# Optimization experiments

Hardware: AMD Instinct MI355X
Metric: run time of the kernel (lower is better)

Reference implementation:

```python
import jax, jax.numpy as jnp
from jax import lax
import numpy as np

T, IN, H, L = 8192, 128, 1024, 3


def setup_inputs() -> dict:
    key = jax.random.key(0)
    ks = jax.random.split(key, 12)
    s = 0.05  # scale params to avoid saturating sigmoid/tanh
    return {
        "S": jax.random.normal(ks[0], (T, IN), jnp.float32),
        "h0": jax.random.normal(ks[1], (L, H), jnp.float32),
        "w_ih0": jax.random.normal(ks[2], (2 * H, IN), jnp.float32) * s,
        "w_hh0": jax.random.normal(ks[3], (2 * H, H), jnp.float32) * s,
        "b_ih0": jax.random.normal(ks[4], (2 * H,), jnp.float32) * s,
        "b_hh0": jax.random.normal(ks[5], (2 * H,), jnp.float32) * s,
        "w_ih_rest": jax.random.normal(ks[6], (L - 1, 2 * H, H), jnp.float32) * s,
        "w_hh_rest": jax.random.normal(ks[7], (L - 1, 2 * H, H), jnp.float32) * s,
        "b_ih_rest": jax.random.normal(ks[8], (L - 1, 2 * H), jnp.float32) * s,
        "b_hh_rest": jax.random.normal(ks[9], (L - 1, 2 * H), jnp.float32) * s,
        "w_out": jax.random.normal(ks[10], (1, H), jnp.float32) * s,
        "b_out": jax.random.normal(ks[11], (1,), jnp.float32) * s,
    }


def _mgu_layer(x_seq, h0, w_ih, w_hh, b_ih, b_hh):
    # Precompute the input projection for all timesteps at once: [T, 2H]
    gi = x_seq @ w_ih.T + b_ih

    def step(h, gi_t):
        gh = h @ w_hh.T + b_hh                      # [2H]
        i_f, i_n = jnp.split(gi_t, 2)
        h_f, h_n = jnp.split(gh, 2)
        f = jax.nn.sigmoid(i_f + h_f)               # forget gate
        n = jnp.tanh(i_n + f * h_n)                 # new candidate
        hy = n + (1.0 - f) * (h - n)
        return hy, hy

    _, out = lax.scan(step, h0, gi)                 # out: [T, H]
    return out


def reference(S, h0, w_ih0, w_hh0, b_ih0, b_hh0,
              w_ih_rest, w_hh_rest, b_ih_rest, b_hh_rest,
              w_out, b_out):
    x = _mgu_layer(S, h0[0], w_ih0, w_hh0, b_ih0, b_hh0)
    for l in range(w_ih_rest.shape[0]):             # fixed small layer count
        x = _mgu_layer(x, h0[l + 1], w_ih_rest[l], w_hh_rest[l],
                       b_ih_rest[l], b_hh_rest[l])
    out = (x @ w_out.T + b_out).reshape(-1)          # [T]
    return out
```

## Files before the change

### kernel.cpp

```cpp
#include <hip/hip_runtime.h>
#include <math.h>
#include <stdint.h>


#define T_STEPS 8192
#define HDIM 1024
#define RING 128

typedef unsigned long long u64;

__device__ __forceinline__ u64 agload64(const u64* p) {
    return __hip_atomic_load(p, __ATOMIC_RELAXED, __HIP_MEMORY_SCOPE_AGENT);
}
__device__ __forceinline__ void agstore64(u64* p, u64 v) {
    __hip_atomic_store(p, v, __ATOMIC_RELAXED, __HIP_MEMORY_SCOPE_AGENT);
}
__device__ __forceinline__ int agloadi(const int* p) {
    return __hip_atomic_load(p, __ATOMIC_RELAXED, __HIP_MEMORY_SCOPE_AGENT);
}
__device__ __forceinline__ void agstorei(int* p, int v) {
    __hip_atomic_store(p, v, __ATOMIC_RELAXED, __HIP_MEMORY_SCOPE_AGENT);
}
__device__ __forceinline__ float dot4(float4 a, float4 b) {
    return a.x * b.x + a.y * b.y + a.z * b.z + a.w * b.w;
}
__device__ __forceinline__ u64 pack(float v, int tag) {
    return ((u64)(unsigned)tag << 32) | (u64)__float_as_uint(v);
}
__device__ __forceinline__ void opaque4(float4& v) {
    asm volatile("" : "+v"(v.x), "+v"(v.y), "+v"(v.z), "+v"(v.w));
}
__device__ __forceinline__ void opaque2(float2& v) {
    asm volatile("" : "+v"(v.x), "+v"(v.y));
}

template <int K, int L>
__device__ void scan_layer(float* __restrict__ s_h,
                           float* __restrict__ s_x,
                           const float* __restrict__ S,
                           const u64*  __restrict__ xring_in,
                           u64*        __restrict__ xring_out,
                           float*      __restrict__ xout,
                           const float* __restrict__ h0,
                           const float* __restrict__ w_ih,
                           const float* __restrict__ b_ih,
                           const float* __restrict__ w_hh,
                           const float* __restrict__ b_hh,
                           u64* __restrict__ htag,
                           int* __restrict__ progNext,
                           int* __restrict__ progSelf,
                           int r)
{
    const int tid = threadIdx.x;
    const int a   = tid >> 6;
    const int q   = tid & 63;
    const int jb  = r * 16 + 2 * a;

    float4 wf[2][4], wn[2][4];
#pragma unroll
    for (int g = 0; g < 2; ++g) {
        const float* rf = w_hh + (size_t)(jb + g) * HDIM;
        const float* rn = w_hh + (size_t)(HDIM + jb + g) * HDIM;
#pragma unroll
        for (int m = 0; m < 4; ++m) {
            wf[g][m] = *(const float4*)(rf + 4 * q + 256 * m);
            wn[g][m] = *(const float4*)(rn + 4 * q + 256 * m);
            opaque4(wf[g][m]); opaque4(wn[g][m]);
        }
    }
    float4 wif[2][4], win[2][4];
    float2 wif2[2], win2[2];
    if constexpr (K == 1024) {
#pragma unroll
        for (int g = 0; g < 2; ++g) {
            const float* rf = w_ih + (size_t)(jb + g) * K;
            const float* rn = w_ih + (size_t)(HDIM + jb + g) * K;
#pragma unroll
            for (int m = 0; m < 4; ++m) {
                wif[g][m] = *(const float4*)(rf + 4 * q + 256 * m);
                win[g][m] = *(const float4*)(rn + 4 * q + 256 * m);
                opaque4(wif[g][m]); opaque4(win[g][m]);
            }
        }
    } else {
#pragma unroll
        for (int g = 0; g < 2; ++g) {
            wif2[g] = *(const float2*)(w_ih + (size_t)(jb + g) * K + 2 * q);
            win2[g] = *(const float2*)(w_ih + (size_t)(HDIM + jb + g) * K + 2 * q);
            opaque2(wif2[g]); opaque2(win2[g]);
        }
    }
    float bFv[2], bInv[2], bHnv[2];
#pragma unroll
    for (int g = 0; g < 2; ++g) {
        bFv[g]  = b_ih[jb + g] + b_hh[jb + g];
        bInv[g] = b_ih[HDIM + jb + g];
        bHnv[g] = b_hh[HDIM + jb + g];
    }

    int lastProg = 0;
    for (int t = 0; t < T_STEPS; ++t) {
        const int par = t & 1;
        const u64* hrow = htag + (size_t)((t + 1) & 1) * HDIM;
        u64*       hpub = htag + (size_t)par * HDIM;
        float* hD = s_h + par * HDIM;
        float* xD = s_x + par * HDIM;

        if constexpr (L < 2) {
            if (t - lastProg > RING - 16) {
                do { lastProg = agloadi(progNext); } while (t - lastProg > RING - 16);
            }
        }

        if (t == 0) {
            hD[tid]       = h0[tid];
            hD[tid + 512] = h0[tid + 512];
        }
        {
            const unsigned he = (unsigned)t;
            const unsigned xe = (unsigned)(t + 1);
            const u64* xrow = (L > 0)
                ? xring_in + (size_t)(t & (RING - 1)) * HDIM : nullptr;
            u64 hw0 = 0, hw1 = 0, xw0 = 0, xw1 = 0;
            bool d0 = (t == 0), d1 = (t == 0);
            bool e0 = (L == 0), e1 = (L == 0);
            while (!(d0 && d1 && e0 && e1)) {
                if (!d0) { hw0 = agload64(hrow + tid);       d0 = ((unsigned)(hw0 >> 32) == he); }
                if (!d1) { hw1 = agload64(hrow + tid + 512); d1 = ((unsigned)(hw1 >> 32) == he); }
                if constexpr (L > 0) {
                    if (!e0) { xw0 = agload64(xrow + tid);       e0 = ((unsigned)(xw0 >> 32) == xe); }
                    if (!e1) { xw1 = agload64(xrow + tid + 512); e1 = ((unsigned)(xw1 >> 32) == xe); }
                }
            }
            if (t > 0) {
                hD[tid]       = __uint_as_float((unsigned)hw0);
                hD[tid + 512] = __uint_as_float((unsigned)hw1);
            }
            if constexpr (L > 0) {
                xD[tid]       = __uint_as_float((unsigned)xw0);
                xD[tid + 512] = __uint_as_float((unsigned)xw1);
            }
        }
        if constexpr (L == 0) {
            if (tid < K / 4)
                ((float4*)xD)[tid] = ((const float4*)(S + (size_t)t * K))[tid];
        }
        __syncthreads();

        if constexpr (L > 0) {
            if (r == 0 && tid == 0) agstorei(progSelf, t + 1);
        }

        float aF[2]  = {0.f, 0.f};
        float aNh[2] = {0.f, 0.f};
        float aNi[2] = {0.f, 0.f};
#pragma unroll
        for (int m = 0; m < 4; ++m) {
            const float4 h4 = ((const float4*)hD)[q + 64 * m];
#pragma unroll
            for (int g = 0; g < 2; ++g) {
                aF[g]  += dot4(wf[g][m], h4);
                aNh[g] += dot4(wn[g][m], h4);
            }
        }
        if constexpr (K == 1024) {
#pragma unroll
            for (int m = 0; m < 4; ++m) {
                const float4 x4 = ((const float4*)xD)[q + 64 * m];
#pragma unroll
                for (int g = 0; g < 2; ++g) {
                    aF[g]  += dot4(wif[g][m], x4);
                    aNi[g] += dot4(win[g][m], x4);
                }
            }
        } else {
            const float2 x2 = *(const float2*)&xD[2 * q];
#pragma unroll
            for (int g = 0; g < 2; ++g) {
                aF[g]  += wif2[g].x * x2.x + wif2[g].y * x2.y;
                aNi[g] += win2[g].x * x2.x + win2[g].y * x2.y;
            }
        }

#pragma unroll
        for (int g = 0; g < 2; ++g) {
            aF[g]  += __shfl_xor(aF[g],  1, 64);
            aNh[g] += __shfl_xor(aNh[g], 1, 64);
            aNi[g] += __shfl_xor(aNi[g], 1, 64);
        }
        const int gs = q & 1;
        float vF  = gs ? aF[1]  : aF[0];
        float vNh = gs ? aNh[1] : aNh[0];
        float vNi = gs ? aNi[1] : aNi[0];
#pragma unroll
        for (int off = 2; off <= 32; off <<= 1) {
            vF  += __shfl_xor(vF,  off, 64);
            vNh += __shfl_xor(vNh, off, 64);
            vNi += __shfl_xor(vNi, off, 64);
        }

        if (q < 2) {
            const float cF  = gs ? bFv[1]  : bFv[0];
            const float cIn = gs ? bInv[1] : bInv[0];
            const float cHn = gs ? bHnv[1] : bHnv[0];
            const int   j   = jb + q;
            const float hp  = hD[j];
            const float f   = 1.f / (1.f + expf(-(vF + cF)));
            const float n   = tanhf(vNi + cIn + f * (vNh + cHn));
            const float hy  = n + (1.f - f) * (hp - n);
            const u64   pk  = pack(hy, t + 1);
            agstore64(hpub + j, pk);
            if constexpr (L < 2) {
                agstore64(xring_out + (size_t)(t & (RING - 1)) * HDIM + j, pk);
            } else {
                xout[(size_t)t * HDIM + j] = hy;
            }
        }
    }
}

__global__ __launch_bounds__(512, 2)
void mgu_pipe(const float* __restrict__ S,
              const float* __restrict__ h0,
              const float* __restrict__ w_ih0, const float* __restrict__ b_ih0,
              const float* __restrict__ w_hh0, const float* __restrict__ b_hh0,
              const float* __restrict__ w_ih_r, const float* __restrict__ b_ih_r,
              const float* __restrict__ w_hh_r, const float* __restrict__ b_hh_r,
              float* __restrict__ xbuf2, u64* __restrict__ ring0,
              u64* __restrict__ ring1, u64* __restrict__ htag,
              int* __restrict__ prog)
{
    __shared__ __align__(16) float s_h[2 * HDIM];
    __shared__ __align__(16) float s_x[2 * HDIM];
    const int grp = blockIdx.x >> 6;
    const int r   = blockIdx.x & 63;
    if (grp == 0) {
        scan_layer<128, 0>(s_h, s_x, S, nullptr, ring0, nullptr, h0,
                           w_ih0, b_ih0, w_hh0, b_hh0,
                           htag, prog + 1, nullptr, r);
    } else if (grp == 1) {
        scan_layer<1024, 1>(s_h, s_x, nullptr, ring0, ring1, nullptr, h0 + HDIM,
                            w_ih_r, b_ih_r, w_hh_r, b_hh_r,
                            htag + 2 * HDIM, prog + 2, prog + 1, r);
    } else {
        scan_layer<1024, 2>(s_h, s_x, nullptr, ring1, nullptr, xbuf2,
                            h0 + 2 * HDIM,
                            w_ih_r + 2048 * 1024, b_ih_r + 2048,
                            w_hh_r + 2048 * 1024, b_hh_r + 2048,
                            htag + 4 * HDIM, nullptr, prog + 2, r);
    }
}

__global__ __launch_bounds__(256)
void mgu_out(const float* __restrict__ x,
             const float* __restrict__ w_out,
             const float* __restrict__ b_out,
             float* __restrict__ out)
{
    const int wave = threadIdx.x >> 6;
    const int lane = threadIdx.x & 63;
    const int t = blockIdx.x * 4 + wave;
    float acc = 0.f;
#pragma unroll
    for (int m = 0; m < 4; ++m) {
        const int i4 = lane + 64 * m;
        const float4 x4 = ((const float4*)(x + (size_t)t * HDIM))[i4];
        const float4 w4 = ((const float4*)w_out)[i4];
        acc += dot4(x4, w4);
    }
#pragma unroll
    for (int off = 32; off > 0; off >>= 1) acc += __shfl_xor(acc, off, 64);
    if (lane == 0) out[t] = acc + b_out[0];
}

extern "C" void kernel_launch(void* const* d_in, const int* in_sizes, int n_in,
                              void* d_out, int out_size, void* d_ws, size_t ws_size,
                              hipStream_t stream) {
    const float* S      = (const float*)d_in[0];
    const float* h0     = (const float*)d_in[1];
    const float* w_ih0  = (const float*)d_in[2];
    const float* w_hh0  = (const float*)d_in[3];
    const float* b_ih0  = (const float*)d_in[4];
    const float* b_hh0  = (const float*)d_in[5];
    const float* w_ih_r = (const float*)d_in[6];
    const float* w_hh_r = (const float*)d_in[7];
    const float* b_ih_r = (const float*)d_in[8];
    const float* b_hh_r = (const float*)d_in[9];
    const float* w_out  = (const float*)d_in[10];
    const float* b_out  = (const float*)d_in[11];
    float* out = (float*)d_out;

    char* ws = (char*)d_ws;
    float* xbuf2 = (float*)(ws);
    u64*   ring0 = (u64*)(ws + (32u << 20));
    u64*   ring1 = (u64*)(ws + (33u << 20));
    u64*   htag  = (u64*)(ws + (34u << 20));
    int*   prog  = (int*)(ws + (34u << 20) + (64u << 10));

    mgu_pipe<<<192, 512, 0, stream>>>(S, h0, w_ih0, b_ih0, w_hh0, b_hh0,
                                      w_ih_r, b_ih_r, w_hh_r, b_hh_r,
                                      xbuf2, ring0, ring1, htag, prog);
    mgu_out<<<2048, 256, 0, stream>>>(xbuf2, w_out, b_out, out);
}
```

Baseline: 23.22 ms.

## Split input projection into separate producer blocks and widen recurrent grid

Layers 1 and 2 no longer compute the input projection inside the recurrent blocks. Dedicated 'army' blocks compute the W_ih·x gate inputs and publish them through tagged ring buffers, so each recurrent block only does the W_hh·h matvec. Each recurrent layer is also spread over 128 blocks of 256 threads instead of 64 blocks of 512, for 512 blocks in total. The aim is to shorten the per-timestep critical path of the serial recurrence, at the cost of more blocks spin-waiting, more cross-block flag traffic, a min-scan over 64 progress counters, and a risk of deadlock if the 512 persistent blocks are not all resident at once.

Result: slower. 25.07 ms (+8.0%).

```diff
diff --git a/kernel.cpp b/kernel.cpp
--- a/kernel.cpp
+++ b/kernel.cpp
@@ -6,6 +6,7 @@
 #define T_STEPS 8192
 #define HDIM 1024
 #define RING 128
+#define SLACK (RING - 16)
 
 typedef unsigned long long u64;
 
@@ -34,192 +35,308 @@
     asm volatile("" : "+v"(v.x), "+v"(v.y));
 }
 
-template <int K, int L>
-__device__ void scan_layer(float* __restrict__ s_h,
-                           float* __restrict__ s_x,
-                           const float* __restrict__ S,
-                           const u64*  __restrict__ xring_in,
-                           u64*        __restrict__ xring_out,
-                           float*      __restrict__ xout,
-                           const float* __restrict__ h0,
+__device__ __forceinline__ int minscan64(const int* parr, int q) {
+    int p = agloadi(parr + q);
+#pragma unroll
+    for (int off = 32; off; off >>= 1) {
+        const int o = __shfl_xor(p, off, 64);
+        p = p < o ? p : o;
+    }
+    return p;
+}
+
+template <int L>
+__device__ void rec_layer(float* __restrict__ s_h,
+                          float* __restrict__ s_x0,
+                          float (*__restrict__ s_gi)[16],
+                          const float* __restrict__ S,
+                          const float* __restrict__ h0,
+                          const float* __restrict__ w_ih,
+                          const float* __restrict__ b_ih,
+                          const float* __restrict__ w_hh,
+                          const float* __restrict__ b_hh,
+                          const u64* __restrict__ giRing,
+                          u64* __restrict__ ring_out,
+                          float* __restrict__ xout,
+                          u64* __restrict__ htag,
+                          const int* __restrict__ progArr,
+                          int* __restrict__ progGiSelf,
+                          int r)
+{
+    const int tid = threadIdx.x;
+    const int a   = tid >> 6;
+    const int q   = tid & 63;
+    const int jb  = r * 8 + 2 * a;
+
+    float4 wf[2][4], wn[2][4];
+#pragma unroll
+    for (int g = 0; g < 2; ++g) {
+        const float* rf = w_hh + (size_t)(jb + g) * HDIM;
+        const float* rn = w_hh + (size_t)(HDIM + jb + g) * HDIM;
+#pragma unroll
+        for (int m = 0; m < 4; ++m) {
+            wf[g][m] = *(const float4*)(rf + 4 * q + 256 * m);
+            wn[g][m] = *(const float4*)(rn + 4 * q + 256 * m);
+            opaque4(wf[g][m]); opaque4(wn[g][m]);
+        }
+    }
+    float2 wif2[2] = {}, win2[2] = {};
+    float bFv[2], bInv[2] = {0.f, 0.f}, bHnv[2];
+    if constexpr (L == 0) {
+#pragma unroll
+        for (int g = 0; g < 2; ++g) {
+            wif2[g] = *(const float2*)(w_ih + (size_t)(jb + g) * 128 + 2 * q);
+            win2[g] = *(const float2*)(w_ih + (size_t)(HDIM + jb + g) * 128 + 2 * q);
+            opaque2(wif2[g]); opaque2(win2[g]);
+            bFv[g]  = b_ih[jb + g] + b_hh[jb + g];
+            bInv[g] = b_ih[HDIM + jb + g];
+            bHnv[g] = b_hh[HDIM + jb + g];
+        }
+    } else {
+#pragma unroll
+        for (int g = 0; g < 2; ++g) {
+            bFv[g]  = b_hh[jb + g];
+            bHnv[g] = b_hh[HDIM + jb + g];
+        }
+    }
+
+    int lastProg = 0;
+
+    for (int t = 0; t < T_STEPS; ++t) {
+        const int par = t & 1;
+        float* hD = s_h + par * HDIM;
+        const u64* hrow = htag + (size_t)((t + 1) & 1) * HDIM;
+        u64*       hpub = htag + (size_t)par * HDIM;
+
+        if constexpr (L < 2) {
+            if (t - lastProg > SLACK) {
+                do { lastProg = minscan64(progArr, q); }
+                while (t - lastProg > SLACK);
+            }
+        }
+
+        if constexpr (L == 0) {
+            float* xD = s_x0 + par * 128;
+            if (tid < 32)
+                ((float4*)xD)[tid] = ((const float4*)(S + (size_t)t * 128))[tid];
+        } else {
+            if (tid < 16) {
+                const unsigned xe = (unsigned)(t + 1);
+                const u64* p = giRing + (size_t)(t & (RING - 1)) * 2048
+                             + (tid < 8 ? (size_t)(8 * r + tid)
+                                        : (size_t)(1024 + 8 * r + (tid - 8)));
+                u64 w;
+                do { w = agload64(p); } while ((unsigned)(w >> 32) != xe);
+                s_gi[par][tid] = __uint_as_float((unsigned)w);
+            }
+        }
+
+        if (t == 0) {
+            hD[tid]       = h0[tid];
+            hD[tid + 256] = h0[tid + 256];
+            hD[tid + 512] = h0[tid + 512];
+            hD[tid + 768] = h0[tid + 768];
+        } else {
+            const unsigned he = (unsigned)t;
+            u64 w0 = 0, w1 = 0, w2 = 0, w3 = 0;
+            bool d0 = false, d1 = false, d2 = false, d3 = false;
+            while (!(d0 && d1 && d2 && d3)) {
+                if (!d0) { w0 = agload64(hrow + tid);       d0 = ((unsigned)(w0 >> 32) == he); }
+                if (!d1) { w1 = agload64(hrow + tid + 256); d1 = ((unsigned)(w1 >> 32) == he); }
+                if (!d2) { w2 = agload64(hrow + tid + 512); d2 = ((unsigned)(w2 >> 32) == he); }
+                if (!d3) { w3 = agload64(hrow + tid + 768); d3 = ((unsigned)(w3 >> 32) == he); }
+            }
+            hD[tid]       = __uint_as_float((unsigned)w0);
+            hD[tid + 256] = __uint_as_float((unsigned)w1);
+            hD[tid + 512] = __uint_as_float((unsigned)w2);
+            hD[tid + 768] = __uint_as_float((unsigned)w3);
+        }
+        __syncthreads();
+
+        if constexpr (L > 0) {
+            if (r == 0 && tid == 0) agstorei(progGiSelf, t + 1);
+        }
+
+        float aF[2]  = {0.f, 0.f};
+        float aNh[2] = {0.f, 0.f};
+        float aNi[2] = {0.f, 0.f};
+#pragma unroll
+        for (int m = 0; m < 4; ++m) {
+            const float4 h4 = ((const float4*)hD)[q + 64 * m];
+#pragma unroll
+            for (int g = 0; g < 2; ++g) {
+                aF[g]  += dot4(wf[g][m], h4);
+                aNh[g] += dot4(wn[g][m], h4);
+            }
+        }
+        if constexpr (L == 0) {
+            const float* xD = s_x0 + par * 128;
+            const float2 x2 = *(const float2*)&xD[2 * q];
+#pragma unroll
+            for (int g = 0; g < 2; ++g) {
+                aF[g]  += wif2[g].x * x2.x + wif2[g].y * x2.y;
+                aNi[g] += win2[g].x * x2.x + win2[g].y * x2.y;
+            }
+        }
+
+#pragma unroll
+        for (int g = 0; g < 2; ++g) {
+            aF[g]  += __shfl_xor(aF[g],  1, 64);
+            aNh[g] += __shfl_xor(aNh[g], 1, 64);
+            if constexpr (L == 0) aNi[g] += __shfl_xor(aNi[g], 1, 64);
+        }
+        const int gsl = q & 1;
+        float vF  = gsl ? aF[1]  : aF[0];
+        float vNh = gsl ? aNh[1] : aNh[0];
+        float vNi = 0.f;
+        if constexpr (L == 0) vNi = gsl ? aNi[1] : aNi[0];
+#pragma unroll
+        for (int off = 2; off <= 32; off <<= 1) {
+            vF  += __shfl_xor(vF,  off, 64);
+            vNh += __shfl_xor(vNh, off, 64);
+            if constexpr (L == 0) vNi += __shfl_xor(vNi, off, 64);
+        }
+
+        if (q < 2) {
+            const int   j  = jb + q;
+            const float hp = hD[j];
+            float f, n;
+            if constexpr (L == 0) {
+                const float cF  = gsl ? bFv[1]  : bFv[0];
+                const float cIn = gsl ? bInv[1] : bInv[0];
+                const float cHn = gsl ? bHnv[1] : bHnv[0];
+                f = 1.f / (1.f + expf(-(vF + cF)));
+                n = tanhf(vNi + cIn + f * (vNh + cHn));
+            } else {
+                const float cHf = gsl ? bFv[1]  : bFv[0];
+                const float cHn = gsl ? bHnv[1] : bHnv[0];
+                const float gf  = s_gi[par][2 * a + q];
+                const float gn  = s_gi[par][8 + 2 * a + q];
+                f = 1.f / (1.f + expf(-(gf + vF + cHf)));
+                n = tanhf(gn + f * (vNh + cHn));
+            }
+            const float hy = n + (1.f - f) * (hp - n);
+            const u64   pk = pack(hy, t + 1);
+            agstore64(hpub + j, pk);
+            if constexpr (L < 2) {
+                agstore64(ring_out + (size_t)(t & (RING - 1)) * HDIM + j, pk);
+            } else {
+                xout[(size_t)t * HDIM + j] = hy;
+            }
+        }
+    }
+}
+
+__device__ void army_layer(float* __restrict__ s_x,
+                           const u64* __restrict__ xring,
+                           u64* __restrict__ giRing,
                            const float* __restrict__ w_ih,
                            const float* __restrict__ b_ih,
-                           const float* __restrict__ w_hh,
-                           const float* __restrict__ b_hh,
-                           u64* __restrict__ htag,
-                           int* __restrict__ progNext,
+                           const int* __restrict__ progGiNext,
                            int* __restrict__ progSelf,
                            int r)
 {
     const int tid = threadIdx.x;
     const int a   = tid >> 6;
     const int q   = tid & 63;
-    const int jb  = r * 16 + 2 * a;
-
-    float4 wf[2][4], wn[2][4];
-#pragma unroll
-    for (int g = 0; g < 2; ++g) {
-        const float* rf = w_hh + (size_t)(jb + g) * HDIM;
-        const float* rn = w_hh + (size_t)(HDIM + jb + g) * HDIM;
+    const int jb  = r * 16 + 4 * a;
+
+    float4 wiF[4][4], wiN[4][4];
+#pragma unroll
+    for (int g = 0; g < 4; ++g) {
+        const float* rf = w_ih + (size_t)(jb + g) * HDIM;
+        const float* rn = w_ih + (size_t)(HDIM + jb + g) * HDIM;
 #pragma unroll
         for (int m = 0; m < 4; ++m) {
-            wf[g][m] = *(const float4*)(rf + 4 * q + 256 * m);
-            wn[g][m] = *(const float4*)(rn + 4 * q + 256 * m);
-            opaque4(wf[g][m]); opaque4(wn[g][m]);
-        }
-    }
-    float4 wif[2][4], win[2][4];
-    float2 wif2[2], win2[2];
-    if constexpr (K == 1024) {
-#pragma unroll
-        for (int g = 0; g < 2; ++g) {
-            const float* rf = w_ih + (size_t)(jb + g) * K;
-            const float* rn = w_ih + (size_t)(HDIM + jb + g) * K;
-#pragma unroll
-            for (int m = 0; m < 4; ++m) {
-                wif[g][m] = *(const float4*)(rf + 4 * q + 256 * m);
-                win[g][m] = *(const float4*)(rn + 4 * q + 256 * m);
-                opaque4(wif[g][m]); opaque4(win[g][m]);
-            }
-        }
-    } else {
-#pragma unroll
-        for (int g = 0; g < 2; ++g) {
-            wif2[g] = *(const float2*)(w_ih + (size_t)(jb + g) * K + 2 * q);
-            win2[g] = *(const float2*)(w_ih + (size_t)(HDIM + jb + g) * K + 2 * q);
-            opaque2(wif2[g]); opaque2(win2[g]);
-        }
-    }
-    float bFv[2], bInv[2], bHnv[2];
-#pragma unroll
-    for (int g = 0; g < 2; ++g) {
-        bFv[g]  = b_ih[jb + g] + b_hh[jb + g];
-        bInv[g] = b_ih[HDIM + jb + g];
-        bHnv[g] = b_hh[HDIM + jb + g];
+            wiF[g][m] = *(const float4*)(rf + 4 * q + 256 * m);
+            wiN[g][m] = *(const float4*)(rn + 4 * q + 256 * m);
+            opaque4(wiF[g][m]); opaque4(wiN[g][m]);
+        }
+    }
+    float bIF[4], bIN[4];
+#pragma unroll
+    for (int g = 0; g < 4; ++g) {
+        bIF[g] = b_ih[jb + g];
+        bIN[g] = b_ih[HDIM + jb + g];
     }
 
     int lastProg = 0;
+
     for (int t = 0; t < T_STEPS; ++t) {
         const int par = t & 1;
-        const u64* hrow = htag + (size_t)((t + 1) & 1) * HDIM;
-        u64*       hpub = htag + (size_t)par * HDIM;
-        float* hD = s_h + par * HDIM;
         float* xD = s_x + par * HDIM;
 
-        if constexpr (L < 2) {
-            if (t - lastProg > RING - 16) {
-                do { lastProg = agloadi(progNext); } while (t - lastProg > RING - 16);
-            }
-        }
-
-        if (t == 0) {
-            hD[tid]       = h0[tid];
-            hD[tid + 512] = h0[tid + 512];
-        }
+        if (t - lastProg > SLACK) {
+            do { lastProg = agloadi(progGiNext); } while (t - lastProg > SLACK);
+        }
+
         {
-            const unsigned he = (unsigned)t;
             const unsigned xe = (unsigned)(t + 1);
-            const u64* xrow = (L > 0)
-                ? xring_in + (size_t)(t & (RING - 1)) * HDIM : nullptr;
-            u64 hw0 = 0, hw1 = 0, xw0 = 0, xw1 = 0;
-            bool d0 = (t == 0), d1 = (t == 0);
-            bool e0 = (L == 0), e1 = (L == 0);
-            while (!(d0 && d1 && e0 && e1)) {
-                if (!d0) { hw0 = agload64(hrow + tid);       d0 = ((unsigned)(hw0 >> 32) == he); }
-                if (!d1) { hw1 = agload64(hrow + tid + 512); d1 = ((unsigned)(hw1 >> 32) == he); }
-                if constexpr (L > 0) {
-                    if (!e0) { xw0 = agload64(xrow + tid);       e0 = ((unsigned)(xw0 >> 32) == xe); }
-                    if (!e1) { xw1 = agload64(xrow + tid + 512); e1 = ((unsigned)(xw1 >> 32) == xe); }
-                }
-            }
-            if (t > 0) {
-                hD[tid]       = __uint_as_float((unsigned)hw0);
-                hD[tid + 512] = __uint_as_float((unsigned)hw1);
-            }
-            if constexpr (L > 0) {
-                xD[tid]       = __uint_as_float((unsigned)xw0);
-                xD[tid + 512] = __uint_as_float((unsigned)xw1);
-            }
-        }
-        if constexpr (L == 0) {
-            if (tid < K / 4)
-                ((float4*)xD)[tid] = ((const float4*)(S + (size_t)t * K))[tid];
+            const u64* xrow = xring + (size_t)(t & (RING - 1)) * HDIM;
+            u64 w0 = 0, w1 = 0, w2 = 0, w3 = 0;
+            bool d0 = false, d1 = false, d2 = false, d3 = false;
+            while (!(d0 && d1 && d2 && d3)) {
+                if (!d0) { w0 = agload64(xrow + tid);       d0 = ((unsigned)(w0 >> 32) == xe); }
+                if (!d1) { w1 = agload64(xrow + tid + 256); d1 = ((unsigned)(w1 >> 32) == xe); }
+                if (!d2) { w2 = agload64(xrow + tid + 512); d2 = ((unsigned)(w2 >> 32) == xe); }
+                if (!d3) { w3 = agload64(xrow + tid + 768); d3 = ((unsigned)(w3 >> 32) == xe); }
+            }
+            xD[tid]       = __uint_as_float((unsigned)w0);
+            xD[tid + 256] = __uint_as_float((unsigned)w1);
+            xD[tid + 512] = __uint_as_float((unsigned)w2);
+            xD[tid + 768] = __uint_as_float((unsigned)w3);
         }
         __syncthreads();
 
-        if constexpr (L > 0) {
-            if (r == 0 && tid == 0) agstorei(progSelf, t + 1);
-        }
-
-        float aF[2]  = {0.f, 0.f};
-        float aNh[2] = {0.f, 0.f};
-        float aNi[2] = {0.f, 0.f};
+        if (tid == 0) agstorei(progSelf, t + 1);
+
+        float aGF[4] = {0.f, 0.f, 0.f, 0.f};
+        float aGN[4] = {0.f, 0.f, 0.f, 0.f};
 #pragma unroll
         for (int m = 0; m < 4; ++m) {
-            const float4 h4 = ((const float4*)hD)[q + 64 * m];
-#pragma unroll
-            for (int g = 0; g < 2; ++g) {
-                aF[g]  += dot4(wf[g][m], h4);
-                aNh[g] += dot4(wn[g][m], h4);
-            }
-        }
-        if constexpr (K == 1024) {
-#pragma unroll
-            for (int m = 0; m < 4; ++m) {
-                const float4 x4 = ((const float4*)xD)[q + 64 * m];
-#pragma unroll
-                for (int g = 0; g < 2; ++g) {
-                    aF[g]  += dot4(wif[g][m], x4);
-                    aNi[g] += dot4(win[g][m], x4);
-                }
-            }
-        } else {
-            const float2 x2 = *(const float2*)&xD[2 * q];
-#pragma unroll
-            for (int g = 0; g < 2; ++g) {
-                aF[g]  += wif2[g].x * x2.x + wif2[g].y * x2.y;
-                aNi[g] += win2[g].x * x2.x + win2[g].y * x2.y;
-            }
-        }
-
-#pragma unroll
-        for (int g = 0; g < 2; ++g) {
-            aF[g]  += __shfl_xor(aF[g],  1, 64);
-            aNh[g] += __shfl_xor(aNh[g], 1, 64);
-            aNi[g] += __shfl_xor(aNi[g], 1, 64);
-        }
-        const int gs = q & 1;
-        float vF  = gs ? aF[1]  : aF[0];
-        float vNh = gs ? aNh[1] : aNh[0];
-        float vNi = gs ? aNi[1] : aNi[0];
-#pragma unroll
-        for (int off = 2; off <= 32; off <<= 1) {
-            vF  += __shfl_xor(vF,  off, 64);
-            vNh += __shfl_xor(vNh, off, 64);
-            vNi += __shfl_xor(vNi, off, 64);
-        }
-
-        if (q < 2) {
-            const float cF  = gs ? bFv[1]  : bFv[0];
-            const float cIn = gs ? bInv[1] : bInv[0];
-            const float cHn = gs ? bHnv[1] : bHnv[0];
-            const int   j   = jb + q;
-            const float hp  = hD[j];
-            const float f   = 1.f / (1.f + expf(-(vF + cF)));
-            const float n   = tanhf(vNi + cIn + f * (vNh + cHn));
-            const float hy  = n + (1.f - f) * (hp - n);
-            const u64   pk  = pack(hy, t + 1);
-            agstore64(hpub + j, pk);
-            if constexpr (L < 2) {
-                agstore64(xring_out + (size_t)(t & (RING - 1)) * HDIM + j, pk);
-            } else {
-                xout[(size_t)t * HDIM + j] = hy;
-            }
-        }
-    }
-}
-
-__global__ __launch_bounds__(512, 2)
+            const float4 x4 = ((const float4*)xD)[q + 64 * m];
+#pragma unroll
+            for (int g = 0; g < 4; ++g) {
+                aGF[g] += dot4(wiF[g][m], x4);
+                aGN[g] += dot4(wiN[g][m], x4);
+            }
+        }
+
+#pragma unroll
+        for (int g = 0; g < 4; ++g) {
+            aGF[g] += __shfl_xor(aGF[g], 1, 64);
+            aGN[g] += __shfl_xor(aGN[g], 1, 64);
+        }
+        const int s1 = q & 1;
+        float bF0 = s1 ? aGF[1] : aGF[0];
+        float bF1 = s1 ? aGF[3] : aGF[2];
+        float bN0 = s1 ? aGN[1] : aGN[0];
+        float bN1 = s1 ? aGN[3] : aGN[2];
+        bF0 += __shfl_xor(bF0, 2, 64);
+        bF1 += __shfl_xor(bF1, 2, 64);
+        bN0 += __shfl_xor(bN0, 2, 64);
+        bN1 += __shfl_xor(bN1, 2, 64);
+        const int s2 = (q >> 1) & 1;
+        float vGF = s2 ? bF1 : bF0;
+        float vGN = s2 ? bN1 : bN0;
+#pragma unroll
+        for (int off = 4; off <= 32; off <<= 1) {
+            vGF += __shfl_xor(vGF, off, 64);
+            vGN += __shfl_xor(vGN, off, 64);
+        }
+
+        if (q < 4) {
+            const int j = jb + q;
+            u64* grow = giRing + (size_t)(t & (RING - 1)) * 2048;
+            const float bf = s1 ? (s2 ? bIF[3] : bIF[1]) : (s2 ? bIF[2] : bIF[0]);
+            const float bn = s1 ? (s2 ? bIN[3] : bIN[1]) : (s2 ? bIN[2] : bIN[0]);
+            agstore64(grow + j,        pack(vGF + bf, t + 1));
+            agstore64(grow + 1024 + j, pack(vGN + bn, t + 1));
+        }
+    }
+}
+
+__global__ __launch_bounds__(256, 2)
 void mgu_pipe(const float* __restrict__ S,
               const float* __restrict__ h0,
               const float* __restrict__ w_ih0, const float* __restrict__ b_ih0,
@@ -227,27 +344,41 @@
               const float* __restrict__ w_ih_r, const float* __restrict__ b_ih_r,
               const float* __restrict__ w_hh_r, const float* __restrict__ b_hh_r,
               float* __restrict__ xbuf2, u64* __restrict__ ring0,
-              u64* __restrict__ ring1, u64* __restrict__ htag,
+              u64* __restrict__ ring1, u64* __restrict__ gi1,
+              u64* __restrict__ gi2, u64* __restrict__ htag,
               int* __restrict__ prog)
 {
     __shared__ __align__(16) float s_h[2 * HDIM];
-    __shared__ __align__(16) float s_x[2 * HDIM];
-    const int grp = blockIdx.x >> 6;
-    const int r   = blockIdx.x & 63;
-    if (grp == 0) {
-        scan_layer<128, 0>(s_h, s_x, S, nullptr, ring0, nullptr, h0,
-                           w_ih0, b_ih0, w_hh0, b_hh0,
-                           htag, prog + 1, nullptr, r);
-    } else if (grp == 1) {
-        scan_layer<1024, 1>(s_h, s_x, nullptr, ring0, ring1, nullptr, h0 + HDIM,
-                            w_ih_r, b_ih_r, w_hh_r, b_hh_r,
-                            htag + 2 * HDIM, prog + 2, prog + 1, r);
+    __shared__ __align__(16) float s_x0[2 * 128];
+    __shared__ float s_gi[2][16];
+
+    int* prog_gi1 = prog + 0;
+    int* prog_gi2 = prog + 16;
+    int* prog_a3  = prog + 64;
+    int* prog_a4  = prog + 128;
+
+    const int bid = blockIdx.x;
+    if (bid < 128) {
+        rec_layer<0>(s_h, s_x0, s_gi, S, h0,
+                     w_ih0, b_ih0, w_hh0, b_hh0,
+                     nullptr, ring0, nullptr,
+                     htag, prog_a3, nullptr, bid);
+    } else if (bid < 256) {
+        rec_layer<1>(s_h, nullptr, s_gi, nullptr, h0 + HDIM,
+                     nullptr, nullptr, w_hh_r, b_hh_r,
+                     gi1, ring1, nullptr,
+                     htag + 2 * HDIM, prog_a4, prog_gi1, bid - 128);
+    } else if (bid < 384) {
+        rec_layer<2>(s_h, nullptr, s_gi, nullptr, h0 + 2 * HDIM,
+                     nullptr, nullptr, w_hh_r + 2048 * 1024, b_hh_r + 2048,
+                     gi2, nullptr, xbuf2,
+                     htag + 4 * HDIM, nullptr, prog_gi2, bid - 256);
+    } else if (bid < 448) {
+        army_layer(s_h, ring0, gi1, w_ih_r, b_ih_r,
+                   prog_gi1, prog_a3 + (bid - 384), bid - 384);
     } else {
-        scan_layer<1024, 2>(s_h, s_x, nullptr, ring1, nullptr, xbuf2,
-                            h0 + 2 * HDIM,
-                            w_ih_r + 2048 * 1024, b_ih_r + 2048,
-                            w_hh_r + 2048 * 1024, b_hh_r + 2048,
-                            htag + 4 * HDIM, nullptr, prog + 2, r);
+        army_layer(s_h, ring1, gi2, w_ih_r + 2048 * 1024, b_ih_r + 2048,
+                   prog_gi2, prog_a4 + (bid - 448), bid - 448);
     }
 }
 
@@ -294,11 +425,14 @@
     float* xbuf2 = (float*)(ws);
     u64*   ring0 = (u64*)(ws + (32u << 20));
     u64*   ring1 = (u64*)(ws + (33u << 20));
-    u64*   htag  = (u64*)(ws + (34u << 20));
-    int*   prog  = (int*)(ws + (34u << 20) + (64u << 10));
-
-    mgu_pipe<<<192, 512, 0, stream>>>(S, h0, w_ih0, b_ih0, w_hh0, b_hh0,
+    u64*   gi1   = (u64*)(ws + (34u << 20));
+    u64*   gi2   = (u64*)(ws + (36u << 20));
+    u64*   htag  = (u64*)(ws + (38u << 20));
+    int*   prog  = (int*)(ws + (38u << 20) + (64u << 10));
+
+    mgu_pipe<<<512, 256, 0, stream>>>(S, h0, w_ih0, b_ih0, w_hh0, b_hh0,
                                       w_ih_r, b_ih_r, w_hh_r, b_hh_r,
-                                      xbuf2, ring0, ring1, htag, prog);
+                                      xbuf2, ring0, ring1, gi1, gi2,
+                                      htag, prog);
     mgu_out<<<2048, 256, 0, stream>>>(xbuf2, w_out, b_out, out);
 }
```
